# Kernel tuning notes

Measured on AMD Instinct MI355X. Metric: run time of the kernel, lower is better.

The kernel has to match this reference:

```python
import jax, jax.numpy as jnp
import numpy as np
import math

M = 100000
K = 27
CIN = 64
COUT = 64


def setup_inputs() -> dict:
    key = jax.random.key(0)
    k1, k2, k3 = jax.random.split(key, 3)
    feats = jax.random.normal(k1, (M, CIN), dtype=jnp.float32)
    # rulebook: indices into feats rows; -1 marks a missing neighbor (~ sparse sites)
    rulebook = jax.random.randint(k2, (M, K), -1, M, dtype=jnp.int64)
    weight = jax.random.normal(k3, (K, CIN, COUT), dtype=jnp.float32) * (1.0 / math.sqrt(CIN))
    bias = jnp.zeros((COUT,), dtype=jnp.float32)
    return {"feats": feats, "rulebook": rulebook, "weight": weight, "bias": bias}


def reference(feats, rulebook, weight, bias):
    # mask invalid (-1) rulebook entries, clamp for a safe gather
    mask = (rulebook >= 0)  # (M, K)
    safe = jnp.clip(rulebook, 0)
    # gather neighbor features per kernel offset: (M, K, Cin)
    gathered = feats[safe] * mask[..., None].astype(feats.dtype)
    # per-offset GEMM fused with the reduce over K: sum_k gathered[m,k,:] @ W[k]
    out = jnp.einsum('mkc,kco->mo', gathered, weight)
    # mean reduce: divide by per-voxel valid-neighbor count
    denom = jnp.clip(mask.sum(axis=1), 1).astype(out.dtype)[:, None]  # (M, 1)
    out = out / denom
    out = out + bias
    # residual (in_ch == out_ch, so identity skip)
    out = out + feats
    return out
```

## Files before the change

### kernel.cpp

```cpp
#include <hip/hip_runtime.h>
#include <hip/hip_bf16.h>

#define NPTS 100000
#define KOFF 27
#define KPAD 28
#define NCH  64

typedef __attribute__((ext_vector_type(4))) float f32x4;
typedef __attribute__((ext_vector_type(4))) unsigned int u32x4;
typedef __attribute__((ext_vector_type(2))) long long2_t;

__global__ void convert_feats_kernel(const float* __restrict__ feats,
                                     unsigned char* __restrict__ f8) {
  int tid = blockIdx.x * 256 + threadIdx.x;
  const int total = (NPTS + 1) * 4;
  if (tid >= total) return;
  const int m  = tid >> 2;
  const int lk = tid & 3;
  unsigned int w0 = 0, w1 = 0, w2 = 0, w3 = 0;
  if (m < NPTS) {
    const float* r = feats + (size_t)m * NCH + lk * 8;
    const float4 a = *reinterpret_cast<const float4*>(r);
    const float4 b = *reinterpret_cast<const float4*>(r + 4);
    const float4 c = *reinterpret_cast<const float4*>(r + 32);
    const float4 d = *reinterpret_cast<const float4*>(r + 36);
    int p;
    p = __builtin_amdgcn_cvt_pk_fp8_f32(a.x, a.y, 0, false);
    p = __builtin_amdgcn_cvt_pk_fp8_f32(a.z, a.w, p, true);  w0 = (unsigned)p;
    p = __builtin_amdgcn_cvt_pk_fp8_f32(b.x, b.y, 0, false);
    p = __builtin_amdgcn_cvt_pk_fp8_f32(b.z, b.w, p, true);  w1 = (unsigned)p;
    p = __builtin_amdgcn_cvt_pk_fp8_f32(c.x, c.y, 0, false);
    p = __builtin_amdgcn_cvt_pk_fp8_f32(c.z, c.w, p, true);  w2 = (unsigned)p;
    p = __builtin_amdgcn_cvt_pk_fp8_f32(d.x, d.y, 0, false);
    p = __builtin_amdgcn_cvt_pk_fp8_f32(d.z, d.w, p, true);  w3 = (unsigned)p;
  }
  *reinterpret_cast<u32x4*>(f8 + (size_t)m * 64 + lk * 16) = u32x4{w0, w1, w2, w3};
}

__global__ void convert_weight_kernel(const float* __restrict__ w,
                                      unsigned char* __restrict__ wt) {
  int tid = blockIdx.x * 256 + threadIdx.x;
  if (tid >= KPAD * NCH * NCH) return;
  int ko  = tid >> 12;
  int rem = tid & 4095;
  int c   = rem >> 6;
  int o   = rem & 63;
  float val = (ko < KOFF) ? w[(size_t)ko * 4096 + c * 64 + o] : 0.0f;
  int p8 = __builtin_amdgcn_cvt_pk_fp8_f32(val, 0.0f, 0, false);
  const int h  = c >> 5;
  const int kk = c & 31;
  const int L  = ((kk >> 3) << 4) | (o & 15);
  int dst = ((ko * 4) + (o >> 4)) * 1024 + L * 16 + h * 8 + (kk & 7);
  wt[dst] = (unsigned char)(p8 & 0xff);
}

__global__ __launch_bounds__(256, 4)
void spconv_kernel(const unsigned char* __restrict__ f8,
                   const int* __restrict__ rulebook,
                   const unsigned char* __restrict__ wl,
                   const float* __restrict__ feats,
                   const float* __restrict__ bias,
                   float* __restrict__ out) {
  __shared__ int s_off[128][KPAD];
  __shared__ int s_cnt[128];

  const int tid = threadIdx.x;
  const int m0  = blockIdx.x * 128;

  if (tid < 128) s_cnt[tid] = 0;
  __syncthreads();

  for (int f = tid; f < 128 * KPAD; f += 256) {
    int r = f / KPAD, k = f - r * KPAD;
    int m = m0 + r;
    int off = NPTS * 64;
    if (m < NPTS && k < KOFF) {
      int v = rulebook[(size_t)m * KOFF + k];
      if (v >= 0) { off = v * 64; atomicAdd(&s_cnt[r], 1); }
    }
    s_off[r][k] = off;
  }
  __syncthreads();

  const int wave = tid >> 6;
  const int lane = tid & 63;
  const int lr   = lane & 15;
  const int lk   = lane >> 4;
  const int lk16 = lk * 16;
  const int row0 = wave * 32 + lr;
  const int row1 = wave * 32 + 16 + lr;

  const char* fbase = (const char*)f8;
  const char* wlane = (const char*)wl + lane * 16;

  f32x4 acc0[4] = {f32x4{0,0,0,0}, f32x4{0,0,0,0}, f32x4{0,0,0,0}, f32x4{0,0,0,0}};
  f32x4 acc1[4] = {f32x4{0,0,0,0}, f32x4{0,0,0,0}, f32x4{0,0,0,0}, f32x4{0,0,0,0}};

  long2_t A0r0, A0r1, A1r0, A1r1;
  long2_t B0, B1, B2, B3;

#define LOADA(R0, R1, KO) {                                                   \
    R0 = *reinterpret_cast<const long2_t*>(fbase + (size_t)(unsigned)s_off[row0][(KO)] + lk16); \
    R1 = *reinterpret_cast<const long2_t*>(fbase + (size_t)(unsigned)s_off[row1][(KO)] + lk16); \
  }

#define LOADB(KO) {                                                           \
    const char* wb_ = wlane + (size_t)(KO) * 4096;                            \
    B0 = *reinterpret_cast<const long2_t*>(wb_ + 0 * 1024);                   \
    B1 = *reinterpret_cast<const long2_t*>(wb_ + 1 * 1024);                   \
    B2 = *reinterpret_cast<const long2_t*>(wb_ + 2 * 1024);                   \
    B3 = *reinterpret_cast<const long2_t*>(wb_ + 3 * 1024);                   \
  }

#define MFMA_STEP(R0, R1) {                                                   \
    acc0[0] = __builtin_amdgcn_mfma_f32_16x16x32_fp8_fp8(R0.x, B0.x, acc0[0],0,0,0);\
    acc0[0] = __builtin_amdgcn_mfma_f32_16x16x32_fp8_fp8(R0.y, B0.y, acc0[0],0,0,0);\
    acc1[0] = __builtin_amdgcn_mfma_f32_16x16x32_fp8_fp8(R1.x, B0.x, acc1[0],0,0,0);\
    acc1[0] = __builtin_amdgcn_mfma_f32_16x16x32_fp8_fp8(R1.y, B0.y, acc1[0],0,0,0);\
    acc0[1] = __builtin_amdgcn_mfma_f32_16x16x32_fp8_fp8(R0.x, B1.x, acc0[1],0,0,0);\
    acc0[1] = __builtin_amdgcn_mfma_f32_16x16x32_fp8_fp8(R0.y, B1.y, acc0[1],0,0,0);\
    acc1[1] = __builtin_amdgcn_mfma_f32_16x16x32_fp8_fp8(R1.x, B1.x, acc1[1],0,0,0);\
    acc1[1] = __builtin_amdgcn_mfma_f32_16x16x32_fp8_fp8(R1.y, B1.y, acc1[1],0,0,0);\
    acc0[2] = __builtin_amdgcn_mfma_f32_16x16x32_fp8_fp8(R0.x, B2.x, acc0[2],0,0,0);\
    acc0[2] = __builtin_amdgcn_mfma_f32_16x16x32_fp8_fp8(R0.y, B2.y, acc0[2],0,0,0);\
    acc1[2] = __builtin_amdgcn_mfma_f32_16x16x32_fp8_fp8(R1.x, B2.x, acc1[2],0,0,0);\
    acc1[2] = __builtin_amdgcn_mfma_f32_16x16x32_fp8_fp8(R1.y, B2.y, acc1[2],0,0,0);\
    acc0[3] = __builtin_amdgcn_mfma_f32_16x16x32_fp8_fp8(R0.x, B3.x, acc0[3],0,0,0);\
    acc0[3] = __builtin_amdgcn_mfma_f32_16x16x32_fp8_fp8(R0.y, B3.y, acc0[3],0,0,0);\
    acc1[3] = __builtin_amdgcn_mfma_f32_16x16x32_fp8_fp8(R1.x, B3.x, acc1[3],0,0,0);\
    acc1[3] = __builtin_amdgcn_mfma_f32_16x16x32_fp8_fp8(R1.y, B3.y, acc1[3],0,0,0);\
  }

  LOADA(A0r0, A0r1, 0)
  LOADA(A1r0, A1r1, 1)
  LOADB(0)

  #pragma unroll 1
  for (int kk = 0; kk < KPAD / 2; ++kk) {
    const int ko = kk * 2;
    MFMA_STEP(A0r0, A0r1)
    LOADB(ko + 1)
    if (ko + 2 < KPAD) LOADA(A0r0, A0r1, ko + 2)
    MFMA_STEP(A1r0, A1r1)
    if (ko + 2 < KPAD) LOADB(ko + 2)
    if (ko + 3 < KPAD) LOADA(A1r0, A1r1, ko + 3)
  }
#undef LOADA
#undef LOADB
#undef MFMA_STEP

  #pragma unroll
  for (int rt = 0; rt < 2; ++rt) {
    #pragma unroll
    for (int nt = 0; nt < 4; ++nt) {
      const int col = nt * 16 + lr;
      const float b = bias[col];
      #pragma unroll
      for (int i = 0; i < 4; ++i) {
        const int rl = wave * 32 + rt * 16 + lk * 4 + i;
        const int m  = m0 + rl;
        if (m < NPTS) {
          const float denom = (float)max(s_cnt[rl], 1);
          const float a = (rt == 0) ? acc0[nt][i] : acc1[nt][i];
          out[(size_t)m * NCH + col] =
              a / denom + b + feats[(size_t)m * NCH + col];
        }
      }
    }
  }
}

extern "C" void kernel_launch(void* const* d_in, const int* in_sizes, int n_in,
                              void* d_out, int out_size, void* d_ws, size_t ws_size,
                              hipStream_t stream) {
  const float* feats    = (const float*)d_in[0];
  const int*   rulebook = (const int*)d_in[1];
  const float* weight   = (const float*)d_in[2];
  const float* bias     = (const float*)d_in[3];
  float* out = (float*)d_out;

  unsigned char* f8 = (unsigned char*)d_ws;
  const size_t f8_bytes = (size_t)(NPTS + 1) * NCH;
  const size_t wt_off   = (f8_bytes + 1023) & ~(size_t)1023;
  unsigned char* wl = (unsigned char*)((char*)d_ws + wt_off);

  {
    const int total = (NPTS + 1) * 4;
    convert_feats_kernel<<<(total + 255) / 256, 256, 0, stream>>>(feats, f8);
  }
  {
    const int n = KPAD * NCH * NCH;
    convert_weight_kernel<<<(n + 255) / 256, 256, 0, stream>>>(weight, wl);
  }
  {
    const int nblk = (NPTS + 127) / 128;
    spconv_kernel<<<nblk, 256, 0, stream>>>(f8, rulebook, wl, feats, bias, out);
  }
}
```

Measured before the change: 70.07 us.

## Deepen gather/MFMA software pipeline with triple-buffered A and paired-offset B loads

The main loop now processes kernel offsets in pairs. Gathered feature rows are triple-buffered, so loads for group G+2 are issued before the MFMAs for group G, and weights for two offsets are double-buffered. A sched_barrier keeps the compiler from moving the gather loads past the MFMA block. Launch bounds are relaxed from 4 to 2 blocks per SM to make room for the extra live registers. The aim is to keep more gather latency in flight per wave, at the cost of lower occupancy.

```diff
diff --git a/kernel.cpp b/kernel.cpp
--- a/kernel.cpp
+++ b/kernel.cpp
@@ -54,7 +54,10 @@
   wt[dst] = (unsigned char)(p8 & 0xff);
 }
 
-__global__ __launch_bounds__(256, 4)
+struct AGrp { long2_t k0r0, k0r1, k1r0, k1r1; };
+struct BGrp { long2_t a0, a1, a2, a3, b0, b1, b2, b3; };
+
+__global__ __launch_bounds__(256, 2)
 void spconv_kernel(const unsigned char* __restrict__ f8,
                    const int* __restrict__ rulebook,
                    const unsigned char* __restrict__ wl,
@@ -92,62 +95,89 @@
 
   const char* fbase = (const char*)f8;
   const char* wlane = (const char*)wl + lane * 16;
+  const int* soff0 = &s_off[row0][0];
+  const int* soff1 = &s_off[row1][0];
 
   f32x4 acc0[4] = {f32x4{0,0,0,0}, f32x4{0,0,0,0}, f32x4{0,0,0,0}, f32x4{0,0,0,0}};
   f32x4 acc1[4] = {f32x4{0,0,0,0}, f32x4{0,0,0,0}, f32x4{0,0,0,0}, f32x4{0,0,0,0}};
 
-  long2_t A0r0, A0r1, A1r0, A1r1;
-  long2_t B0, B1, B2, B3;
-
-#define LOADA(R0, R1, KO) {                                                   \
-    R0 = *reinterpret_cast<const long2_t*>(fbase + (size_t)(unsigned)s_off[row0][(KO)] + lk16); \
-    R1 = *reinterpret_cast<const long2_t*>(fbase + (size_t)(unsigned)s_off[row1][(KO)] + lk16); \
-  }
-
-#define LOADB(KO) {                                                           \
-    const char* wb_ = wlane + (size_t)(KO) * 4096;                            \
-    B0 = *reinterpret_cast<const long2_t*>(wb_ + 0 * 1024);                   \
-    B1 = *reinterpret_cast<const long2_t*>(wb_ + 1 * 1024);                   \
-    B2 = *reinterpret_cast<const long2_t*>(wb_ + 2 * 1024);                   \
-    B3 = *reinterpret_cast<const long2_t*>(wb_ + 3 * 1024);                   \
-  }
-
-#define MFMA_STEP(R0, R1) {                                                   \
-    acc0[0] = __builtin_amdgcn_mfma_f32_16x16x32_fp8_fp8(R0.x, B0.x, acc0[0],0,0,0);\
-    acc0[0] = __builtin_amdgcn_mfma_f32_16x16x32_fp8_fp8(R0.y, B0.y, acc0[0],0,0,0);\
-    acc1[0] = __builtin_amdgcn_mfma_f32_16x16x32_fp8_fp8(R1.x, B0.x, acc1[0],0,0,0);\
-    acc1[0] = __builtin_amdgcn_mfma_f32_16x16x32_fp8_fp8(R1.y, B0.y, acc1[0],0,0,0);\
-    acc0[1] = __builtin_amdgcn_mfma_f32_16x16x32_fp8_fp8(R0.x, B1.x, acc0[1],0,0,0);\
-    acc0[1] = __builtin_amdgcn_mfma_f32_16x16x32_fp8_fp8(R0.y, B1.y, acc0[1],0,0,0);\
-    acc1[1] = __builtin_amdgcn_mfma_f32_16x16x32_fp8_fp8(R1.x, B1.x, acc1[1],0,0,0);\
-    acc1[1] = __builtin_amdgcn_mfma_f32_16x16x32_fp8_fp8(R1.y, B1.y, acc1[1],0,0,0);\
-    acc0[2] = __builtin_amdgcn_mfma_f32_16x16x32_fp8_fp8(R0.x, B2.x, acc0[2],0,0,0);\
-    acc0[2] = __builtin_amdgcn_mfma_f32_16x16x32_fp8_fp8(R0.y, B2.y, acc0[2],0,0,0);\
-    acc1[2] = __builtin_amdgcn_mfma_f32_16x16x32_fp8_fp8(R1.x, B2.x, acc1[2],0,0,0);\
-    acc1[2] = __builtin_amdgcn_mfma_f32_16x16x32_fp8_fp8(R1.y, B2.y, acc1[2],0,0,0);\
-    acc0[3] = __builtin_amdgcn_mfma_f32_16x16x32_fp8_fp8(R0.x, B3.x, acc0[3],0,0,0);\
-    acc0[3] = __builtin_amdgcn_mfma_f32_16x16x32_fp8_fp8(R0.y, B3.y, acc0[3],0,0,0);\
-    acc1[3] = __builtin_amdgcn_mfma_f32_16x16x32_fp8_fp8(R1.x, B3.x, acc1[3],0,0,0);\
-    acc1[3] = __builtin_amdgcn_mfma_f32_16x16x32_fp8_fp8(R1.y, B3.y, acc1[3],0,0,0);\
-  }
-
-  LOADA(A0r0, A0r1, 0)
-  LOADA(A1r0, A1r1, 1)
-  LOADB(0)
+  AGrp A0, A1, A2;
+  BGrp B0, B1;
+
+#define LOADA(AG, G) {                                                        \
+    AG.k0r0 = *reinterpret_cast<const long2_t*>(fbase + (size_t)(unsigned)soff0[2*(G)]     + lk16); \
+    AG.k0r1 = *reinterpret_cast<const long2_t*>(fbase + (size_t)(unsigned)soff1[2*(G)]     + lk16); \
+    AG.k1r0 = *reinterpret_cast<const long2_t*>(fbase + (size_t)(unsigned)soff0[2*(G) + 1] + lk16); \
+    AG.k1r1 = *reinterpret_cast<const long2_t*>(fbase + (size_t)(unsigned)soff1[2*(G) + 1] + lk16); \
+  }
+
+#define LOADB(BG, G) {                                                        \
+    const char* wb_ = wlane + (size_t)(2*(G)) * 4096;                         \
+    BG.a0 = *reinterpret_cast<const long2_t*>(wb_ + 0 * 1024);                \
+    BG.a1 = *reinterpret_cast<const long2_t*>(wb_ + 1 * 1024);                \
+    BG.a2 = *reinterpret_cast<const long2_t*>(wb_ + 2 * 1024);                \
+    BG.a3 = *reinterpret_cast<const long2_t*>(wb_ + 3 * 1024);                \
+    BG.b0 = *reinterpret_cast<const long2_t*>(wb_ + 4096 + 0 * 1024);         \
+    BG.b1 = *reinterpret_cast<const long2_t*>(wb_ + 4096 + 1 * 1024);         \
+    BG.b2 = *reinterpret_cast<const long2_t*>(wb_ + 4096 + 2 * 1024);         \
+    BG.b3 = *reinterpret_cast<const long2_t*>(wb_ + 4096 + 3 * 1024);         \
+  }
+
+#define MFMA_KO(R0, R1, F0, F1, F2, F3) {                                     \
+    acc0[0] = __builtin_amdgcn_mfma_f32_16x16x32_fp8_fp8(R0.x, F0.x, acc0[0],0,0,0);\
+    acc0[0] = __builtin_amdgcn_mfma_f32_16x16x32_fp8_fp8(R0.y, F0.y, acc0[0],0,0,0);\
+    acc1[0] = __builtin_amdgcn_mfma_f32_16x16x32_fp8_fp8(R1.x, F0.x, acc1[0],0,0,0);\
+    acc1[0] = __builtin_amdgcn_mfma_f32_16x16x32_fp8_fp8(R1.y, F0.y, acc1[0],0,0,0);\
+    acc0[1] = __builtin_amdgcn_mfma_f32_16x16x32_fp8_fp8(R0.x, F1.x, acc0[1],0,0,0);\
+    acc0[1] = __builtin_amdgcn_mfma_f32_16x16x32_fp8_fp8(R0.y, F1.y, acc0[1],0,0,0);\
+    acc1[1] = __builtin_amdgcn_mfma_f32_16x16x32_fp8_fp8(R1.x, F1.x, acc1[1],0,0,0);\
+    acc1[1] = __builtin_amdgcn_mfma_f32_16x16x32_fp8_fp8(R1.y, F1.y, acc1[1],0,0,0);\
+    acc0[2] = __builtin_amdgcn_mfma_f32_16x16x32_fp8_fp8(R0.x, F2.x, acc0[2],0,0,0);\
+    acc0[2] = __builtin_amdgcn_mfma_f32_16x16x32_fp8_fp8(R0.y, F2.y, acc0[2],0,0,0);\
+    acc1[2] = __builtin_amdgcn_mfma_f32_16x16x32_fp8_fp8(R1.x, F2.x, acc1[2],0,0,0);\
+    acc1[2] = __builtin_amdgcn_mfma_f32_16x16x32_fp8_fp8(R1.y, F2.y, acc1[2],0,0,0);\
+    acc0[3] = __builtin_amdgcn_mfma_f32_16x16x32_fp8_fp8(R0.x, F3.x, acc0[3],0,0,0);\
+    acc0[3] = __builtin_amdgcn_mfma_f32_16x16x32_fp8_fp8(R0.y, F3.y, acc0[3],0,0,0);\
+    acc1[3] = __builtin_amdgcn_mfma_f32_16x16x32_fp8_fp8(R1.x, F3.x, acc1[3],0,0,0);\
+    acc1[3] = __builtin_amdgcn_mfma_f32_16x16x32_fp8_fp8(R1.y, F3.y, acc1[3],0,0,0);\
+  }
+
+#define ITER(G, AUSE, ANXT, BUSE) {                                           \
+    LOADA(ANXT, (G) + 2)                                                      \
+    __builtin_amdgcn_sched_barrier(0);                                        \
+    MFMA_KO(AUSE.k0r0, AUSE.k0r1, BUSE.a0, BUSE.a1, BUSE.a2, BUSE.a3)         \
+    MFMA_KO(AUSE.k1r0, AUSE.k1r1, BUSE.b0, BUSE.b1, BUSE.b2, BUSE.b3)         \
+    LOADB(BUSE, (G) + 2)                                                      \
+  }
+
+#define ITER_TAIL(AUSE, BUSE) {                                               \
+    MFMA_KO(AUSE.k0r0, AUSE.k0r1, BUSE.a0, BUSE.a1, BUSE.a2, BUSE.a3)         \
+    MFMA_KO(AUSE.k1r0, AUSE.k1r1, BUSE.b0, BUSE.b1, BUSE.b2, BUSE.b3)         \
+  }
+
+  LOADA(A0, 0)
+  LOADA(A1, 1)
+  LOADB(B0, 0)
+  LOADB(B1, 1)
 
   #pragma unroll 1
-  for (int kk = 0; kk < KPAD / 2; ++kk) {
-    const int ko = kk * 2;
-    MFMA_STEP(A0r0, A0r1)
-    LOADB(ko + 1)
-    if (ko + 2 < KPAD) LOADA(A0r0, A0r1, ko + 2)
-    MFMA_STEP(A1r0, A1r1)
-    if (ko + 2 < KPAD) LOADB(ko + 2)
-    if (ko + 3 < KPAD) LOADA(A1r0, A1r1, ko + 3)
-  }
+  for (int half = 0; half < 2; ++half) {
+    const int g = half * 6;
+    ITER(g + 0, A0, A2, B0)
+    ITER(g + 1, A1, A0, B1)
+    ITER(g + 2, A2, A1, B0)
+    ITER(g + 3, A0, A2, B1)
+    ITER(g + 4, A1, A0, B0)
+    ITER(g + 5, A2, A1, B1)
+  }
+  ITER_TAIL(A0, B0)
+  ITER_TAIL(A1, B1)
+
 #undef LOADA
 #undef LOADB
-#undef MFMA_STEP
+#undef MFMA_KO
+#undef ITER
+#undef ITER_TAIL
 
   #pragma unroll
   for (int rt = 0; rt < 2; ++rt) {
```

New measurement: 76.29 us. +8.9%, slower.
